# Performance work log

Measured on AMD Instinct MI355X. Metric: run time of the kernel, lower is better.

Reference implementation:

```python
import jax, jax.numpy as jnp
import numpy as np

B, NQ, NK, QS, KS, H, VD = 16, 64, 512, 256, 256, 256, 256


def setup_inputs() -> dict:
    key = jax.random.key(0)
    k1, k2, k3, k4, k5, k6, k7 = jax.random.split(key, 7)
    return {
        "queries": jax.random.normal(k1, (B, NQ, QS), dtype=jnp.float32),
        "keys": jax.random.normal(k2, (B, NK, KS), dtype=jnp.float32),
        "values": jax.random.normal(k3, (B, NK, VD), dtype=jnp.float32),
        "valid_lens": jax.random.randint(k4, (B,), 1, NK + 1, dtype=jnp.int32),
        # learned params (nn.Linear with bias=False): W_q [QS,H], W_k [KS,H], w_v [H]
        "W_q": jax.random.normal(k5, (QS, H), dtype=jnp.float32) / np.sqrt(QS),
        "W_k": jax.random.normal(k6, (KS, H), dtype=jnp.float32) / np.sqrt(KS),
        "w_v": jax.random.normal(k7, (H,), dtype=jnp.float32) / np.sqrt(H),
    }


def reference(queries, keys, values, valid_lens, W_q, W_k, w_v):
    # project: q [B,nq,H], k [B,nk,H]
    q = jnp.einsum("bqd,dh->bqh", queries, W_q)
    k = jnp.einsum("bkd,dh->bkh", keys, W_k)
    # broadcast-add -> tanh -> score reduction via w_v: [B,nq,nk]
    features = jnp.tanh(q[:, :, None, :] + k[:, None, :, :])  # [B,nq,nk,H]
    scores = jnp.einsum("bqkh,h->bqk", features, w_v)
    # masked softmax over keys (positions >= valid_len masked out)
    mask = jnp.arange(scores.shape[-1])[None, None, :] < valid_lens[:, None, None]
    scores = jnp.where(mask, scores, -1e6)
    attn = jax.nn.softmax(scores, axis=-1)
    # weighted sum of values (dropout p=0 / eval mode => identity)
    return jnp.einsum("bqk,bkv->bqv", attn, values)
```

## Files before the change

### kernel.cpp

```cpp
#include <hip/hip_runtime.h>
#include <hip/hip_bf16.h>

#define BB 16
#define NQ 64
#define NK 512
#define HD 256

typedef __attribute__((ext_vector_type(8))) short short8;
typedef __attribute__((ext_vector_type(4))) float f32x4;

__device__ __forceinline__ ushort bf16_rne(float v) {
    unsigned u = __float_as_uint(v);
    return (ushort)((u + 0x7FFFu + ((u >> 16) & 1u)) >> 16);
}
__device__ __forceinline__ float bf16_to_f(ushort h) {
    return __uint_as_float(((unsigned)h) << 16);
}

__global__ __launch_bounds__(256) void wconv(
    const float* __restrict__ wq, const float* __restrict__ wk,
    ushort* __restrict__ wqh, ushort* __restrict__ wql,
    ushort* __restrict__ wkh, ushort* __restrict__ wkl)
{
    int widx = blockIdx.x * 256 + threadIdx.x;
    const float* W; ushort *wh, *wl;
    if (widx < 16384) { W = wq; wh = wqh; wl = wql; }
    else { W = wk; wh = wkh; wl = wkl; widx -= 16384; }
    int n  = widx >> 6;
    int k4 = (widx & 63) * 4;
    ushort hh[4], ll[4];
    #pragma unroll
    for (int c = 0; c < 4; ++c) {
        float v = W[(k4 + c) * 256 + n];
        hh[c] = bf16_rne(v);
        ll[c] = bf16_rne(v - bf16_to_f(hh[c]));
    }
    *(ushort4*)&wh[n * 256 + k4] = make_ushort4(hh[0], hh[1], hh[2], hh[3]);
    *(ushort4*)&wl[n * 256 + k4] = make_ushort4(ll[0], ll[1], ll[2], ll[3]);
}

__global__ __launch_bounds__(256, 2) void proj_fused(
    const float* __restrict__ queries, const float* __restrict__ keys,
    const ushort* __restrict__ wqh, const ushort* __restrict__ wql,
    const ushort* __restrict__ wkh, const ushort* __restrict__ wkl,
    float* __restrict__ qp, float* __restrict__ kp, float scale)
{
    __shared__ ushort AsH[64 * 64], AsL[64 * 64];
    __shared__ ushort BsH[64 * 64], BsL[64 * 64];

    const float* A; const ushort *Bh, *Bl; float* C; int rows0;
    const int bx = blockIdx.x;
    if (bx < 16) { A = queries; Bh = wqh; Bl = wql; C = qp; rows0 = bx * 64; }
    else         { A = keys;    Bh = wkh; Bl = wkl; C = kp; rows0 = (bx - 16) * 64; }
    const int cols0 = blockIdx.y * 64;

    const int t = threadIdx.x, lane = t & 63, wave = t >> 6;
    const int quad = lane >> 4, l15 = lane & 15;
    const int sr  = t >> 2;
    const int sc2 = (t & 3) * 2;

    f32x4 acc[4];
    #pragma unroll
    for (int j = 0; j < 4; ++j) acc[j] = (f32x4){0.f, 0.f, 0.f, 0.f};

    for (int k0 = 0; k0 < 256; k0 += 64) {
        const float* arow = &A[(size_t)(rows0 + sr) * 256 + k0 + sc2 * 8];
        float4 a0 = *(const float4*)&arow[0];
        float4 a1 = *(const float4*)&arow[4];
        float4 a2 = *(const float4*)&arow[8];
        float4 a3 = *(const float4*)&arow[12];
        const ushort* bhp = &Bh[(size_t)(cols0 + sr) * 256 + k0 + sc2 * 8];
        const ushort* blp = &Bl[(size_t)(cols0 + sr) * 256 + k0 + sc2 * 8];
        short8 b0h = *(const short8*)&bhp[0];
        short8 b1h = *(const short8*)&bhp[8];
        short8 b0l = *(const short8*)&blp[0];
        short8 b1l = *(const short8*)&blp[8];

        __syncthreads();

        float av[16] = {a0.x, a0.y, a0.z, a0.w, a1.x, a1.y, a1.z, a1.w,
                        a2.x, a2.y, a2.z, a2.w, a3.x, a3.y, a3.z, a3.w};
        short8 ah0, ah1, al0, al1;
        #pragma unroll
        for (int e = 0; e < 8; ++e) {
            ushort h0 = bf16_rne(av[e]);
            ushort h1 = bf16_rne(av[8 + e]);
            ah0[e] = (short)h0;
            ah1[e] = (short)h1;
            al0[e] = (short)bf16_rne(av[e] - bf16_to_f(h0));
            al1[e] = (short)bf16_rne(av[8 + e] - bf16_to_f(h1));
        }
        {
            int s0 = sr * 8 + ((sc2 + 0) ^ (sr & 7));
            int s1 = sr * 8 + ((sc2 + 1) ^ (sr & 7));
            *(short8*)&AsH[s0 * 8] = ah0;
            *(short8*)&AsH[s1 * 8] = ah1;
            *(short8*)&AsL[s0 * 8] = al0;
            *(short8*)&AsL[s1 * 8] = al1;
            *(short8*)&BsH[s0 * 8] = b0h;
            *(short8*)&BsH[s1 * 8] = b1h;
            *(short8*)&BsL[s0 * 8] = b0l;
            *(short8*)&BsL[s1 * 8] = b1l;
        }
        __syncthreads();

        #pragma unroll
        for (int ks = 0; ks < 2; ++ks) {
            const int c = ks * 4 + quad;
            short8 aH, aL, bH[4], bL[4];
            {
                int r = wave * 16 + l15;
                int slot = r * 8 + (c ^ (r & 7));
                aH = *(const short8*)&AsH[slot * 8];
                aL = *(const short8*)&AsL[slot * 8];
            }
            #pragma unroll
            for (int ns = 0; ns < 4; ++ns) {
                int n = ns * 16 + l15;
                int slot = n * 8 + (c ^ (n & 7));
                bH[ns] = *(const short8*)&BsH[slot * 8];
                bL[ns] = *(const short8*)&BsL[slot * 8];
            }
            #pragma unroll
            for (int ns = 0; ns < 4; ++ns)
                acc[ns] = __builtin_amdgcn_mfma_f32_16x16x32_bf16(aH, bH[ns], acc[ns], 0, 0, 0);
            #pragma unroll
            for (int ns = 0; ns < 4; ++ns)
                acc[ns] = __builtin_amdgcn_mfma_f32_16x16x32_bf16(aL, bH[ns], acc[ns], 0, 0, 0);
            #pragma unroll
            for (int ns = 0; ns < 4; ++ns)
                acc[ns] = __builtin_amdgcn_mfma_f32_16x16x32_bf16(aH, bL[ns], acc[ns], 0, 0, 0);
        }
    }

    const int rbase = rows0 + wave * 16 + quad * 4;
    #pragma unroll
    for (int ns = 0; ns < 4; ++ns) {
        int col = cols0 + ns * 16 + l15;
        #pragma unroll
        for (int r = 0; r < 4; ++r)
            C[(size_t)(rbase + r) * 256 + col] = acc[ns][r] * scale;
    }
}

__global__ __launch_bounds__(256) void score_pv_seg3(
    const float* __restrict__ qp,
    const float* __restrict__ kp,
    const float* __restrict__ values,
    const int*   __restrict__ vlens,
    const float* __restrict__ w_v,
    float* __restrict__ pO,
    float* __restrict__ pM,
    float* __restrict__ pL)
{
    __shared__ float eq[8][260];
    __shared__ float wv[HD];
    __shared__ float Ps[8][68];

    const int b   = blockIdx.x & 15;
    const int qt  = blockIdx.x >> 4;
    const int seg = blockIdx.y;
    const int vl  = vlens[b];
    if (seg * 64 >= vl) return;

    const int t = threadIdx.x, lane = t & 63, wave = t >> 6;

    const float* qsrc = qp + ((size_t)b * NQ + qt * 8) * HD;
    #pragma unroll
    for (int i = 0; i < 2; ++i) {
        int idx = i * 256 + t;
        int row = idx >> 6, c4 = (idx & 63) * 4;
        float4 v = *(const float4*)&qsrc[(size_t)row * HD + c4];
        eq[row][c4 + 0] = __builtin_amdgcn_exp2f(v.x);
        eq[row][c4 + 1] = __builtin_amdgcn_exp2f(v.y);
        eq[row][c4 + 2] = __builtin_amdgcn_exp2f(v.z);
        eq[row][c4 + 3] = __builtin_amdgcn_exp2f(v.w);
    }
    if (t < 64) *(float4*)&wv[t * 4] = *(const float4*)&w_v[t * 4];
    __syncthreads();

    float Wsum;
    {
        float ws = wv[lane] + wv[lane + 64] + wv[lane + 128] + wv[lane + 192];
        #pragma unroll
        for (int off = 32; off; off >>= 1) ws += __shfl_xor(ws, off);
        Wsum = ws;
    }

    const int key = wave * 16 + (lane >> 2);
    const int ch  = lane & 3;
    const int kg  = seg * 64 + key;
    const float* krow = kp + ((size_t)b * NK + kg) * HD + ch * 4;

    float s[8] = {0.f, 0.f, 0.f, 0.f, 0.f, 0.f, 0.f, 0.f};
    for (int j4 = 0; j4 < 4; ++j4) {
        float4 kk[4];
        #pragma unroll
        for (int u = 0; u < 4; ++u)
            kk[u] = *(const float4*)&krow[(j4 * 4 + u) * 16];
        #pragma unroll
        for (int u = 0; u < 4; ++u) {
            const int h = (j4 * 4 + u) * 16 + ch * 4;
            float4 w4 = *(const float4*)&wv[h];
            float ek0 = __builtin_amdgcn_exp2f(kk[u].x);
            float ek1 = __builtin_amdgcn_exp2f(kk[u].y);
            float ek2 = __builtin_amdgcn_exp2f(kk[u].z);
            float ek3 = __builtin_amdgcn_exp2f(kk[u].w);
            #pragma unroll
            for (int qi = 0; qi < 8; ++qi) {
                float4 q4 = *(const float4*)&eq[qi][h];
                float t0 = fmaf(w4.x, __builtin_amdgcn_rcpf(fmaf(q4.x, ek0, 1.f)), s[qi]);
                t0 = fmaf(w4.y, __builtin_amdgcn_rcpf(fmaf(q4.y, ek1, 1.f)), t0);
                t0 = fmaf(w4.z, __builtin_amdgcn_rcpf(fmaf(q4.z, ek2, 1.f)), t0);
                s[qi] = fmaf(w4.w, __builtin_amdgcn_rcpf(fmaf(q4.w, ek3, 1.f)), t0);
            }
        }
    }
    #pragma unroll
    for (int qi = 0; qi < 8; ++qi) {
        s[qi] += __shfl_xor(s[qi], 1);
        s[qi] += __shfl_xor(s[qi], 2);
    }
    if (ch == 0) {
        const bool masked = (kg >= vl);
        #pragma unroll
        for (int qi = 0; qi < 8; ++qi)
            Ps[qi][key] = masked ? -1e6f : fmaf(-2.f, s[qi], Wsum);
    }
    __syncthreads();

    const float L2E = 1.4426950408889634f;
    #pragma unroll
    for (int r = 0; r < 2; ++r) {
        const int row = wave * 2 + r;
        float sv = Ps[row][lane];
        float m = sv;
        #pragma unroll
        for (int off = 32; off; off >>= 1) m = fmaxf(m, __shfl_xor(m, off));
        float e = __builtin_amdgcn_exp2f((sv - m) * L2E);
        float l = e;
        #pragma unroll
        for (int off = 32; off; off >>= 1) l += __shfl_xor(l, off);
        Ps[row][lane] = e;
        if (lane == 0) {
            size_t mi = (((size_t)(b * 8 + qt) * 8 + seg)) * 8 + row;
            pM[mi] = m;
            pL[mi] = l;
        }
    }
    __syncthreads();

    const int r0 = wave * 2, r1 = r0 + 1;
    f32x4 acc0 = (f32x4){0.f, 0.f, 0.f, 0.f};
    f32x4 acc1 = (f32x4){0.f, 0.f, 0.f, 0.f};
    const float* vbase = values + ((size_t)b * NK + seg * 64) * HD;
    #pragma unroll 2
    for (int i0 = 0; i0 < 64; i0 += 4) {
        float4 v[4];
        #pragma unroll
        for (int u = 0; u < 4; ++u)
            v[u] = *(const float4*)&vbase[(size_t)(i0 + u) * HD + lane * 4];
        #pragma unroll
        for (int u = 0; u < 4; ++u) {
            float p0 = Ps[r0][i0 + u];
            float p1 = Ps[r1][i0 + u];
            acc0[0] = fmaf(p0, v[u].x, acc0[0]);
            acc0[1] = fmaf(p0, v[u].y, acc0[1]);
            acc0[2] = fmaf(p0, v[u].z, acc0[2]);
            acc0[3] = fmaf(p0, v[u].w, acc0[3]);
            acc1[0] = fmaf(p1, v[u].x, acc1[0]);
            acc1[1] = fmaf(p1, v[u].y, acc1[1]);
            acc1[2] = fmaf(p1, v[u].z, acc1[2]);
            acc1[3] = fmaf(p1, v[u].w, acc1[3]);
        }
    }
    const size_t ob = (((size_t)(b * 8 + qt) * 8 + seg)) * 8 * 256;
    *(f32x4*)&pO[ob + (size_t)r0 * 256 + lane * 4] = acc0;
    *(f32x4*)&pO[ob + (size_t)r1 * 256 + lane * 4] = acc1;
}

__global__ __launch_bounds__(256) void combine_seg2(
    const float* __restrict__ pO, const float* __restrict__ pM,
    const float* __restrict__ pL, const int* __restrict__ vlens,
    float* __restrict__ out)
{
    const int b  = blockIdx.x >> 6;
    const int q  = blockIdx.x & 63;
    const int t  = threadIdx.x;
    const int vl = vlens[b];
    const int nc = (vl + 63) >> 6;
    const int qt = q >> 3, qi = q & 7;
    const float L2E = 1.4426950408889634f;

    const size_t base = (size_t)(b * 8 + qt) * 8;

    float mi[8], li[8];
    float m = -3e38f;
    #pragma unroll
    for (int i = 0; i < 8; ++i) {
        if (i < nc) {
            mi[i] = pM[(base + i) * 8 + qi];
            li[i] = pL[(base + i) * 8 + qi];
            m = fmaxf(m, mi[i]);
        }
    }
    float L = 0.f, wi[8];
    #pragma unroll
    for (int i = 0; i < 8; ++i) {
        if (i < nc) {
            wi[i] = __builtin_amdgcn_exp2f((mi[i] - m) * L2E);
            L = fmaf(li[i], wi[i], L);
        }
    }
    float acc = 0.f;
    #pragma unroll
    for (int i = 0; i < 8; ++i) {
        if (i < nc) acc = fmaf(wi[i], pO[((base + i) * 8 + qi) * 256 + t], acc);
    }
    out[((size_t)(b * 64 + q)) * 256 + t] = acc * __builtin_amdgcn_rcpf(L);
}

extern "C" void kernel_launch(void* const* d_in, const int* in_sizes, int n_in,
                              void* d_out, int out_size, void* d_ws, size_t ws_size,
                              hipStream_t stream) {
    const float* queries = (const float*)d_in[0];
    const float* keys    = (const float*)d_in[1];
    const float* values  = (const float*)d_in[2];
    const int*   vlens   = (const int*)d_in[3];
    const float* W_q     = (const float*)d_in[4];
    const float* W_k     = (const float*)d_in[5];
    const float* w_v     = (const float*)d_in[6];
    float* out = (float*)d_out;

    float*  kp  = (float*)d_ws;
    float*  qp  = kp + (size_t)BB * NK * HD;
    float*  pO  = qp + (size_t)BB * NQ * HD;
    float*  pM  = pO + (size_t)BB * 8 * 8 * 8 * 256;
    float*  pL  = pM + (size_t)BB * 8 * 8 * 8;
    ushort* wqh = (ushort*)(pL + (size_t)BB * 8 * 8 * 8);
    ushort* wql = wqh + 65536;
    ushort* wkh = wql + 65536;
    ushort* wkl = wkh + 65536;

    const float SC = 2.885390081777927f;

    wconv<<<dim3(128), 256, 0, stream>>>(W_q, W_k, wqh, wql, wkh, wkl);
    proj_fused<<<dim3(144, 4), 256, 0, stream>>>(queries, keys,
                                                 wqh, wql, wkh, wkl,
                                                 qp, kp, SC);
    score_pv_seg3<<<dim3(128, 8), 256, 0, stream>>>(qp, kp, values, vlens, w_v,
                                                    pO, pM, pL);
    combine_seg2<<<dim3(BB * NQ), 256, 0, stream>>>(pO, pM, pL, vlens, out);
}
```

Baseline: 115.9 us.

## Fold weight conversion into projection and fuse split-K combine via atomic counter

Drops the separate weight bf16 hi/lo conversion kernel. Each projection block now reads fp32 W columns directly, splits them into hi/lo parts itself and writes them into shared memory. The combine kernel is also removed: the last segment block for each (batch, query-tile) detects it finished last through an atomic counter and threadfence, then merges the partial results for 8 queries. Together this cuts two launches, but every projection block now repeats the weight conversion with strided column reads. The serial merge in the last block also adds tail latency.

```diff
diff --git a/kernel.cpp b/kernel.cpp
--- a/kernel.cpp
+++ b/kernel.cpp
@@ -17,47 +17,30 @@
     return __uint_as_float(((unsigned)h) << 16);
 }
 
-__global__ __launch_bounds__(256) void wconv(
-    const float* __restrict__ wq, const float* __restrict__ wk,
-    ushort* __restrict__ wqh, ushort* __restrict__ wql,
-    ushort* __restrict__ wkh, ushort* __restrict__ wkl)
+__global__ __launch_bounds__(256, 2) void proj_all(
+    const float* __restrict__ queries, const float* __restrict__ keys,
+    const float* __restrict__ W_q, const float* __restrict__ W_k,
+    float* __restrict__ qp, float* __restrict__ kp, float scale,
+    int* __restrict__ cnt)
 {
-    int widx = blockIdx.x * 256 + threadIdx.x;
-    const float* W; ushort *wh, *wl;
-    if (widx < 16384) { W = wq; wh = wqh; wl = wql; }
-    else { W = wk; wh = wkh; wl = wkl; widx -= 16384; }
-    int n  = widx >> 6;
-    int k4 = (widx & 63) * 4;
-    ushort hh[4], ll[4];
-    #pragma unroll
-    for (int c = 0; c < 4; ++c) {
-        float v = W[(k4 + c) * 256 + n];
-        hh[c] = bf16_rne(v);
-        ll[c] = bf16_rne(v - bf16_to_f(hh[c]));
-    }
-    *(ushort4*)&wh[n * 256 + k4] = make_ushort4(hh[0], hh[1], hh[2], hh[3]);
-    *(ushort4*)&wl[n * 256 + k4] = make_ushort4(ll[0], ll[1], ll[2], ll[3]);
-}
-
-__global__ __launch_bounds__(256, 2) void proj_fused(
-    const float* __restrict__ queries, const float* __restrict__ keys,
-    const ushort* __restrict__ wqh, const ushort* __restrict__ wql,
-    const ushort* __restrict__ wkh, const ushort* __restrict__ wkl,
-    float* __restrict__ qp, float* __restrict__ kp, float scale)
-{
+    if (blockIdx.x == 0 && blockIdx.y == 0 && threadIdx.x < 128)
+        cnt[threadIdx.x] = 0;
+
     __shared__ ushort AsH[64 * 64], AsL[64 * 64];
-    __shared__ ushort BsH[64 * 64], BsL[64 * 64];
-
-    const float* A; const ushort *Bh, *Bl; float* C; int rows0;
+    __shared__ ushort WtH[64 * 64], WtL[64 * 64];
+
+    const float* A; const float* W; float* C; int rows0;
     const int bx = blockIdx.x;
-    if (bx < 16) { A = queries; Bh = wqh; Bl = wql; C = qp; rows0 = bx * 64; }
-    else         { A = keys;    Bh = wkh; Bl = wkl; C = kp; rows0 = (bx - 16) * 64; }
+    if (bx < 16) { A = queries; W = W_q; C = qp; rows0 = bx * 64; }
+    else         { A = keys;    W = W_k; C = kp; rows0 = (bx - 16) * 64; }
     const int cols0 = blockIdx.y * 64;
 
     const int t = threadIdx.x, lane = t & 63, wave = t >> 6;
     const int quad = lane >> 4, l15 = lane & 15;
     const int sr  = t >> 2;
     const int sc2 = (t & 3) * 2;
+    const int wn  = t & 63;
+    const int wkc = t >> 6;
 
     f32x4 acc[4];
     #pragma unroll
@@ -69,38 +52,50 @@
         float4 a1 = *(const float4*)&arow[4];
         float4 a2 = *(const float4*)&arow[8];
         float4 a3 = *(const float4*)&arow[12];
-        const ushort* bhp = &Bh[(size_t)(cols0 + sr) * 256 + k0 + sc2 * 8];
-        const ushort* blp = &Bl[(size_t)(cols0 + sr) * 256 + k0 + sc2 * 8];
-        short8 b0h = *(const short8*)&bhp[0];
-        short8 b1h = *(const short8*)&bhp[8];
-        short8 b0l = *(const short8*)&blp[0];
-        short8 b1l = *(const short8*)&blp[8];
+        float wr[2][8];
+        #pragma unroll
+        for (int g = 0; g < 2; ++g) {
+            const int kchunk = wkc + g * 4;
+            #pragma unroll
+            for (int j = 0; j < 8; ++j)
+                wr[g][j] = W[(size_t)(k0 + kchunk * 8 + j) * 256 + cols0 + wn];
+        }
 
         __syncthreads();
 
-        float av[16] = {a0.x, a0.y, a0.z, a0.w, a1.x, a1.y, a1.z, a1.w,
-                        a2.x, a2.y, a2.z, a2.w, a3.x, a3.y, a3.z, a3.w};
-        short8 ah0, ah1, al0, al1;
-        #pragma unroll
-        for (int e = 0; e < 8; ++e) {
-            ushort h0 = bf16_rne(av[e]);
-            ushort h1 = bf16_rne(av[8 + e]);
-            ah0[e] = (short)h0;
-            ah1[e] = (short)h1;
-            al0[e] = (short)bf16_rne(av[e] - bf16_to_f(h0));
-            al1[e] = (short)bf16_rne(av[8 + e] - bf16_to_f(h1));
-        }
         {
+            float av[16] = {a0.x, a0.y, a0.z, a0.w, a1.x, a1.y, a1.z, a1.w,
+                            a2.x, a2.y, a2.z, a2.w, a3.x, a3.y, a3.z, a3.w};
+            short8 ah0, ah1, al0, al1;
+            #pragma unroll
+            for (int e = 0; e < 8; ++e) {
+                ushort h0 = bf16_rne(av[e]);
+                ushort h1 = bf16_rne(av[8 + e]);
+                ah0[e] = (short)h0;
+                ah1[e] = (short)h1;
+                al0[e] = (short)bf16_rne(av[e] - bf16_to_f(h0));
+                al1[e] = (short)bf16_rne(av[8 + e] - bf16_to_f(h1));
+            }
             int s0 = sr * 8 + ((sc2 + 0) ^ (sr & 7));
             int s1 = sr * 8 + ((sc2 + 1) ^ (sr & 7));
             *(short8*)&AsH[s0 * 8] = ah0;
             *(short8*)&AsH[s1 * 8] = ah1;
             *(short8*)&AsL[s0 * 8] = al0;
             *(short8*)&AsL[s1 * 8] = al1;
-            *(short8*)&BsH[s0 * 8] = b0h;
-            *(short8*)&BsH[s1 * 8] = b1h;
-            *(short8*)&BsL[s0 * 8] = b0l;
-            *(short8*)&BsL[s1 * 8] = b1l;
+        }
+        #pragma unroll
+        for (int g = 0; g < 2; ++g) {
+            const int kchunk = wkc + g * 4;
+            short8 h8, l8;
+            #pragma unroll
+            for (int j = 0; j < 8; ++j) {
+                ushort h = bf16_rne(wr[g][j]);
+                h8[j] = (short)h;
+                l8[j] = (short)bf16_rne(wr[g][j] - bf16_to_f(h));
+            }
+            int slot = wn * 8 + (kchunk ^ (wn & 7));
+            *(short8*)&WtH[slot * 8] = h8;
+            *(short8*)&WtL[slot * 8] = l8;
         }
         __syncthreads();
 
@@ -118,8 +113,8 @@
             for (int ns = 0; ns < 4; ++ns) {
                 int n = ns * 16 + l15;
                 int slot = n * 8 + (c ^ (n & 7));
-                bH[ns] = *(const short8*)&BsH[slot * 8];
-                bL[ns] = *(const short8*)&BsL[slot * 8];
+                bH[ns] = *(const short8*)&WtH[slot * 8];
+                bL[ns] = *(const short8*)&WtL[slot * 8];
             }
             #pragma unroll
             for (int ns = 0; ns < 4; ++ns)
@@ -143,25 +138,24 @@
     }
 }
 
-__global__ __launch_bounds__(256) void score_pv_seg3(
-    const float* __restrict__ qp,
-    const float* __restrict__ kp,
-    const float* __restrict__ values,
-    const int*   __restrict__ vlens,
+__global__ __launch_bounds__(256) void score_pv_fused(
+    const float* __restrict__ qp, const float* __restrict__ kp,
+    const float* __restrict__ values, const int* __restrict__ vlens,
     const float* __restrict__ w_v,
-    float* __restrict__ pO,
-    float* __restrict__ pM,
-    float* __restrict__ pL)
+    float* __restrict__ pO, float* __restrict__ pM, float* __restrict__ pL,
+    int* __restrict__ cnt, float* __restrict__ out)
 {
     __shared__ float eq[8][260];
     __shared__ float wv[HD];
     __shared__ float Ps[8][68];
+    __shared__ int isLast;
 
     const int b   = blockIdx.x & 15;
     const int qt  = blockIdx.x >> 4;
     const int seg = blockIdx.y;
     const int vl  = vlens[b];
     if (seg * 64 >= vl) return;
+    const int nc  = (vl + 63) >> 6;
 
     const int t = threadIdx.x, lane = t & 63, wave = t >> 6;
 
@@ -277,47 +271,44 @@
     const size_t ob = (((size_t)(b * 8 + qt) * 8 + seg)) * 8 * 256;
     *(f32x4*)&pO[ob + (size_t)r0 * 256 + lane * 4] = acc0;
     *(f32x4*)&pO[ob + (size_t)r1 * 256 + lane * 4] = acc1;
-}
-
-__global__ __launch_bounds__(256) void combine_seg2(
-    const float* __restrict__ pO, const float* __restrict__ pM,
-    const float* __restrict__ pL, const int* __restrict__ vlens,
-    float* __restrict__ out)
-{
-    const int b  = blockIdx.x >> 6;
-    const int q  = blockIdx.x & 63;
-    const int t  = threadIdx.x;
-    const int vl = vlens[b];
-    const int nc = (vl + 63) >> 6;
-    const int qt = q >> 3, qi = q & 7;
-    const float L2E = 1.4426950408889634f;
+
+    __threadfence();
+    if (t == 0) {
+        int old = atomicAdd(&cnt[b * 8 + qt], 1);
+        isLast = (old == nc - 1) ? 1 : 0;
+    }
+    __syncthreads();
+    if (!isLast) return;
+    __threadfence();
 
     const size_t base = (size_t)(b * 8 + qt) * 8;
-
-    float mi[8], li[8];
-    float m = -3e38f;
-    #pragma unroll
-    for (int i = 0; i < 8; ++i) {
-        if (i < nc) {
-            mi[i] = pM[(base + i) * 8 + qi];
-            li[i] = pL[(base + i) * 8 + qi];
-            m = fmaxf(m, mi[i]);
-        }
-    }
-    float L = 0.f, wi[8];
-    #pragma unroll
-    for (int i = 0; i < 8; ++i) {
-        if (i < nc) {
-            wi[i] = __builtin_amdgcn_exp2f((mi[i] - m) * L2E);
-            L = fmaf(li[i], wi[i], L);
-        }
-    }
-    float acc = 0.f;
-    #pragma unroll
-    for (int i = 0; i < 8; ++i) {
-        if (i < nc) acc = fmaf(wi[i], pO[((base + i) * 8 + qi) * 256 + t], acc);
-    }
-    out[((size_t)(b * 64 + q)) * 256 + t] = acc * __builtin_amdgcn_rcpf(L);
+    #pragma unroll
+    for (int qi = 0; qi < 8; ++qi) {
+        float mi[8], li[8];
+        float m = -3e38f;
+        #pragma unroll
+        for (int i = 0; i < 8; ++i) {
+            if (i < nc) {
+                mi[i] = pM[(base + i) * 8 + qi];
+                li[i] = pL[(base + i) * 8 + qi];
+                m = fmaxf(m, mi[i]);
+            }
+        }
+        float L = 0.f, wi[8];
+        #pragma unroll
+        for (int i = 0; i < 8; ++i) {
+            if (i < nc) {
+                wi[i] = __builtin_amdgcn_exp2f((mi[i] - m) * L2E);
+                L = fmaf(li[i], wi[i], L);
+            }
+        }
+        float acc = 0.f;
+        #pragma unroll
+        for (int i = 0; i < 8; ++i) {
+            if (i < nc) acc = fmaf(wi[i], pO[((base + i) * 8 + qi) * 256 + t], acc);
+        }
+        out[((size_t)(b * 64 + qt * 8 + qi)) * 256 + t] = acc * __builtin_amdgcn_rcpf(L);
+    }
 }
 
 extern "C" void kernel_launch(void* const* d_in, const int* in_sizes, int n_in,
@@ -332,23 +323,17 @@
     const float* w_v     = (const float*)d_in[6];
     float* out = (float*)d_out;
 
-    float*  kp  = (float*)d_ws;
-    float*  qp  = kp + (size_t)BB * NK * HD;
-    float*  pO  = qp + (size_t)BB * NQ * HD;
-    float*  pM  = pO + (size_t)BB * 8 * 8 * 8 * 256;
-    float*  pL  = pM + (size_t)BB * 8 * 8 * 8;
-    ushort* wqh = (ushort*)(pL + (size_t)BB * 8 * 8 * 8);
-    ushort* wql = wqh + 65536;
-    ushort* wkh = wql + 65536;
-    ushort* wkl = wkh + 65536;
+    float* kp = (float*)d_ws;
+    float* qp = kp + (size_t)BB * NK * HD;
+    float* pO = qp + (size_t)BB * NQ * HD;
+    float* pM = pO + (size_t)BB * 8 * 8 * 8 * 256;
+    float* pL = pM + (size_t)BB * 8 * 8 * 8;
+    int*   cnt = (int*)(pL + (size_t)BB * 8 * 8 * 8);
 
     const float SC = 2.885390081777927f;
 
-    wconv<<<dim3(128), 256, 0, stream>>>(W_q, W_k, wqh, wql, wkh, wkl);
-    proj_fused<<<dim3(144, 4), 256, 0, stream>>>(queries, keys,
-                                                 wqh, wql, wkh, wkl,
-                                                 qp, kp, SC);
-    score_pv_seg3<<<dim3(128, 8), 256, 0, stream>>>(qp, kp, values, vlens, w_v,
-                                                    pO, pM, pL);
-    combine_seg2<<<dim3(BB * NQ), 256, 0, stream>>>(pO, pM, pL, vlens, out);
-}
+    proj_all<<<dim3(144, 4), 256, 0, stream>>>(queries, keys, W_q, W_k,
+                                               qp, kp, SC, cnt);
+    score_pv_fused<<<dim3(128, 8), 256, 0, stream>>>(qp, kp, values, vlens, w_v,
+                                                     pO, pM, pL, cnt, out);
+}
```

Result: slower. 193.8 us (+67.2%).
